# Performance work log

Hardware: AMD Instinct MI355X
Metric: run time of the kernel (lower is better)

Reference implementation:

```python
import jax, jax.numpy as jnp
import numpy as np
from jax import lax

IMG = 1280.0          # image side (80 * stride 16)
HF = WF = 80          # feature map
STRIDE = 16
A = 15                # anchors per location (5 sizes x 3 ratios)
KMIX = 5              # MDN mixture components
NIMG = 8
NGT = 32
PRE_NMS = 2000
POST_NMS = 1000
NMS_THRESH = 0.7
BATCH_PER_IMG = 256
POS_FRAC = 0.5
SCALE_CLAMP = float(np.log(1000.0 / 16.0))
LOG2PI = float(np.log(2.0 * np.pi))


def _make_anchors():
    sizes = np.array([32., 64., 128., 256., 512.])
    ratios = np.array([0.5, 1.0, 2.0])
    ws = (sizes[:, None] * np.sqrt(1.0 / ratios)[None, :]).reshape(-1)
    hs = (sizes[:, None] * np.sqrt(ratios)[None, :]).reshape(-1)
    base = np.stack([-ws / 2, -hs / 2, ws / 2, hs / 2], 1)  # [A,4]
    xs = (np.arange(WF) + 0.5) * STRIDE
    ys = (np.arange(HF) + 0.5) * STRIDE
    sx, sy = np.meshgrid(xs, ys)
    shifts = np.stack([sx.ravel(), sy.ravel(), sx.ravel(), sy.ravel()], 1)  # [HW,4]
    return jnp.asarray((shifts[:, None, :] + base[None]).reshape(-1, 4), jnp.float32)


def setup_inputs() -> dict:
    key = jax.random.key(0)
    k = jax.random.split(key, 6)
    R = HF * WF * A
    anchors = _make_anchors()                                                # [R,4]
    pi = jax.random.normal(k[0], (NIMG, KMIX, R), jnp.float32)
    mu = jax.random.normal(k[1], (NIMG, KMIX, R), jnp.float32)
    sigma = jax.random.uniform(k[2], (NIMG, KMIX, R), jnp.float32, 0.1, 1.0)
    deltas = jax.random.normal(k[3], (NIMG, R, 4), jnp.float32) * 0.1
    xy = jax.random.uniform(k[4], (NIMG, NGT, 2), jnp.float32, 0.0, 960.0)
    wh = jax.random.uniform(k[5], (NIMG, NGT, 2), jnp.float32, 20.0, 320.0)
    gt_boxes = jnp.concatenate([xy, xy + wh], -1)                            # [N,G,4]
    return {"anchors": anchors, "pi": pi, "mu": mu, "sigma": sigma,
            "deltas": deltas, "gt_boxes": gt_boxes}


def pairwise_iou(a, b):  # [M,4],[P,4] -> [M,P]
    area_a = (a[:, 2] - a[:, 0]) * (a[:, 3] - a[:, 1])
    area_b = (b[:, 2] - b[:, 0]) * (b[:, 3] - b[:, 1])
    lt = jnp.maximum(a[:, None, :2], b[None, :, :2])
    rb = jnp.minimum(a[:, None, 2:], b[None, :, 2:])
    wh = jnp.clip(rb - lt, 0.0)
    inter = wh[..., 0] * wh[..., 1]
    return inter / jnp.maximum(area_a[:, None] + area_b[None, :] - inter, 1e-9)


def apply_deltas(d, boxes):  # Box2BoxTransform.apply_deltas, weights=(1,1,1,1)
    w = boxes[:, 2] - boxes[:, 0]
    h = boxes[:, 3] - boxes[:, 1]
    cx = boxes[:, 0] + 0.5 * w
    cy = boxes[:, 1] + 0.5 * h
    dx, dy = d[:, 0], d[:, 1]
    dw = jnp.minimum(d[:, 2], SCALE_CLAMP)
    dh = jnp.minimum(d[:, 3], SCALE_CLAMP)
    pcx = dx * w + cx
    pcy = dy * h + cy
    pw = jnp.exp(dw) * w
    ph = jnp.exp(dh) * h
    return jnp.stack([pcx - 0.5 * pw, pcy - 0.5 * ph, pcx + 0.5 * pw, pcy + 0.5 * ph], 1)


def get_deltas(src, tgt):  # Box2BoxTransform.get_deltas
    sw = src[..., 2] - src[..., 0]
    sh = src[..., 3] - src[..., 1]
    scx = src[..., 0] + 0.5 * sw
    scy = src[..., 1] + 0.5 * sh
    tw = tgt[..., 2] - tgt[..., 0]
    th = tgt[..., 3] - tgt[..., 1]
    tcx = tgt[..., 0] + 0.5 * tw
    tcy = tgt[..., 1] + 0.5 * th
    return jnp.stack([(tcx - scx) / sw, (tcy - scy) / sh,
                      jnp.log(tw / sw), jnp.log(th / sh)], -1)


def _nms_image(boxes, scores, unc):  # [R,4],[R],[R,2] -> padded top proposals
    top_s, tidx = lax.top_k(scores, PRE_NMS)
    tb = jnp.clip(boxes[tidx], 0.0, IMG)   # clip to image
    tu = unc[tidx]
    iou = pairwise_iou(tb, tb)             # [PRE,PRE]
    ar = jnp.arange(PRE_NMS)

    def body(i, keep):
        sup = (iou[i] > NMS_THRESH) & (ar > i) & keep[i]
        return keep & ~sup

    keep = lax.fori_loop(0, PRE_NMS, body, jnp.ones((PRE_NMS,), bool))
    wv = tb[:, 2] - tb[:, 0]
    hv = tb[:, 3] - tb[:, 1]
    keep = keep & (wv > 0.0) & (hv > 0.0)  # min_box_size = 0
    ms = jnp.where(keep, top_s, -jnp.inf)
    out_s, oidx = lax.top_k(ms, POST_NMS)
    return tb[oidx], out_s, tu[oidx]


def _losses(anchors, pi, mu, sigma, deltas, gt_boxes):
    # label_and_sample_anchors (no_grad in torch)
    iou = lax.stop_gradient(jax.vmap(lambda g: pairwise_iou(g, anchors))(gt_boxes))  # [N,G,R]
    vals = iou.max(axis=1)                       # matched IoU quality  [N,R]
    idx = jnp.argmax(iou, axis=1)                # matched gt index     [N,R]
    labels = jnp.where(vals >= 0.7, 1, jnp.where(vals >= 0.3, -1, 0))
    best_gt = iou.max(axis=2)                    # [N,G]
    lq = jnp.any((iou >= best_gt[:, :, None] - 1e-7) & (best_gt[:, :, None] > 0), axis=1)
    labels = jnp.where(lq, 1, labels)            # allow_low_quality_matches
    # deterministic subsample to batch_size_per_image with positive_fraction
    pos = labels == 1
    neg = labels == 0
    n_pos = jnp.minimum(pos.sum(1), int(BATCH_PER_IMG * POS_FRAC))
    keep_pos = pos & (jnp.cumsum(pos, 1) <= n_pos[:, None])
    keep_neg = neg & (jnp.cumsum(neg, 1) <= (BATCH_PER_IMG - n_pos)[:, None])
    labels = jnp.where(keep_pos, 1, jnp.where(keep_neg, 0, -1))
    matched_gt = lax.stop_gradient(jax.vmap(lambda g, i: g[i])(gt_boxes, idx))  # [N,R,4]
    gt_deltas = get_deltas(lax.stop_gradient(anchors)[None], matched_gt)
    pos_mask = labels == 1
    # smooth_l1 with beta=0 -> L1, summed over positives
    loss_loc = jnp.sum(jnp.abs(deltas - gt_deltas) * pos_mask[..., None])
    valid = labels != -1
    t = jnp.clip(vals, 0.0, 1.0)
    lp = jax.nn.log_softmax(pi, axis=1)
    comp = lp - 0.5 * ((t[:, None, :] - mu) / sigma) ** 2 - jnp.log(sigma) - 0.5 * LOG2PI
    nll = -jax.nn.logsumexp(comp, axis=1)        # [N,R]
    loss_cls = jnp.sum(nll * valid)
    norm = BATCH_PER_IMG * pi.shape[0]
    return jnp.stack([loss_cls / norm, loss_loc / norm])


def reference(anchors, pi, mu, sigma, deltas, gt_boxes):
    # find_logit: pi-weighted mixture mean as objectness score
    pi_sm = jax.nn.softmax(pi, axis=1)           # [N,K,R]
    logits = jnp.sum(pi_sm * mu, axis=1)         # [N,R]
    # mdn_uncertainties: epistemic / aleatoric
    epis = jnp.sum(pi_sm * (mu - logits[:, None, :]) ** 2, axis=1)
    alea = jnp.sum(pi_sm * sigma ** 2, axis=1)
    unc = jnp.stack([epis, alea], -1)            # [N,R,2]
    # _decode_proposals
    boxes = jax.vmap(lambda d: apply_deltas(d, anchors))(deltas)  # [N,R,4]
    # find_top_rpn_proposals_uncertainty (pre-NMS topk, clip, NMS, post-NMS topk)
    prop_b, prop_s, prop_u = jax.vmap(_nms_image)(boxes, logits, unc)
    losses = _losses(anchors, pi, mu, sigma, deltas, gt_boxes)    # [loss_cls, loss_loc]
    return prop_b, prop_s, prop_u, losses
```

## Files before the change

kernel.cpp:

```cpp
#include <hip/hip_runtime.h>
#include <cstdint>
#include <cstddef>

typedef unsigned long long u64;
typedef unsigned int u32;
typedef unsigned short u16;
typedef unsigned char u8;

#define R_ANCH 96000
#define NIMG   8
#define KMIX   5
#define PRE    2000
#define POST   1000
#define NGT    32
#define NCHUNK 375
#define NBLK   48
#define MROW   2048
#define GC_STRIDE 16
#define SCAP   16
#define BIG_TH 64

#define IMG_SZ        1280.0f
#define NMS_T         0.7f
#define SCALE_CLAMP_F 4.135166556742356f
#define HALF_L2PI     0.9189385332046727f

__device__ __forceinline__ u64 make_key(float s, int r) {
  u32 u = __float_as_uint(s);
  u = (u & 0x80000000u) ? ~u : (u | 0x80000000u);
  return ((u64)u << 32) | (u64)(0xFFFFFFFFu - (u32)r);
}

__device__ __forceinline__ float dec_score(u64 key) {
  u32 o = (u32)(key >> 32);
  u32 bits = (o & 0x80000000u) ? (o ^ 0x80000000u) : ~o;
  return __uint_as_float(bits);
}

__device__ __forceinline__ float iou_pair(float a0,float a1,float a2,float a3,
                                          float b0,float b1,float b2,float b3) {
#pragma clang fp contract(off)
  float areaA = (a2-a0)*(a3-a1);
  float areaB = (b2-b0)*(b3-b1);
  float lx=fmaxf(a0,b0), ly=fmaxf(a1,b1);
  float rx=fminf(a2,b2), ry=fminf(a3,b3);
  float iw=fmaxf(rx-lx,0.0f), ih=fmaxf(ry-ly,0.0f);
  float inter=iw*ih;
  return inter / fmaxf(areaA+areaB-inter, 1e-9f);
}

__device__ __forceinline__ void pick2048(const u32* __restrict__ hist, int k,
                                         int* s_i, u32* s_u,
                                         int& d_out, int& k_out, u32& cnt_out) {
  int tid = threadIdx.x;
  int lane = tid & 63, w = tid >> 6;
  u32 h[8]; u32 ssum = 0;
#pragma unroll
  for (int i=0;i<8;++i){ h[i] = hist[2047 - (tid*8 + i)]; ssum += h[i]; }
  u32 incl = ssum;
  for (int off=1; off<64; off<<=1){
    u32 t = (u32)__shfl_up((int)incl, off, 64);
    if (lane >= off) incl += t;
  }
  if (lane==63) s_i[w] = (int)incl;
  __syncthreads();
  u32 base = 0;
  for (int ww=0; ww<w; ++ww) base += (u32)s_i[ww];
  u32 run = base + incl - ssum;
#pragma unroll
  for (int i=0;i<8;++i){
    u32 nr = run + h[i];
    if (run < (u32)k && nr >= (u32)k){
      s_u[0] = (u32)(2047 - (tid*8+i));
      s_u[1] = (u32)k - run;
      s_u[2] = h[i];
    }
    run = nr;
  }
  __syncthreads();
  d_out = (int)s_u[0]; k_out = (int)s_u[1]; cnt_out = s_u[2];
  __syncthreads();
}

__device__ __forceinline__ void scan2048_desc(const u32* __restrict__ h,
                                              u32* __restrict__ off,
                                              u32* __restrict__ wsum, int tid) {
  int b_hi = 2047 - 2*tid, b_lo = b_hi - 1;
  u32 h_hi = h[b_hi], h_lo = h[b_lo];
  u32 sum = h_hi + h_lo;
  u32 incl = sum;
  int lane = tid & 63, wv = tid >> 6;
  for (int o=1; o<64; o<<=1){
    u32 t = (u32)__shfl_up((int)incl, o, 64);
    if (lane >= o) incl += t;
  }
  if (lane==63) wsum[wv] = incl;
  __syncthreads();
  u32 base = 0;
  for (int w=0; w<wv; ++w) base += wsum[w];
  u32 excl = base + incl - sum;
  off[b_hi] = excl;
  off[b_lo] = excl + h_hi;
}

__global__ void kZero(u32* z, int nwords) {
  for (int i = blockIdx.x*256 + threadIdx.x; i < nwords; i += gridDim.x*256)
    z[i] = 0u;
}

__global__ __launch_bounds__(256) void kA_mdn(
    const float* __restrict__ pi, const float* __restrict__ mu,
    const float* __restrict__ sigma, float* __restrict__ logits,
    float* __restrict__ epis, float* __restrict__ alea,
    u32* __restrict__ hist0,
    const float* __restrict__ anchors, const float* __restrict__ gt,
    const float* __restrict__ deltas,
    float* __restrict__ nll_o, float* __restrict__ loc_o) {
  __shared__ u32 s_h[2048];
  __shared__ float s_gt[NGT*4];
  int tid = threadIdx.x;
  int r = blockIdx.x*256 + tid;
  int img = blockIdx.y;
  for (int b=tid; b<2048; b+=256) s_h[b]=0u;
  if (tid < NGT*4) s_gt[tid] = gt[img*NGT*4 + tid];
  size_t base = (size_t)img*KMIX*R_ANCH + r;
  float p[KMIX], m[KMIX], s[KMIX];
#pragma unroll
  for (int k=0;k<KMIX;k++){
    p[k]=pi[base+(size_t)k*R_ANCH];
    m[k]=mu[base+(size_t)k*R_ANCH];
    s[k]=sigma[base+(size_t)k*R_ANCH];
  }
  float mx = p[0];
#pragma unroll
  for (int k=1;k<KMIX;k++) mx = fmaxf(mx,p[k]);
  float e[KMIX]; float sum = 0.0f;
#pragma unroll
  for (int k=0;k<KMIX;k++){ e[k]=expf(p[k]-mx); sum += e[k]; }
  float w[KMIX]; float lg = 0.0f;
#pragma unroll
  for (int k=0;k<KMIX;k++){ w[k]=e[k]/sum; lg += w[k]*m[k]; }
  float ep = 0.0f, al = 0.0f;
#pragma unroll
  for (int k=0;k<KMIX;k++){ float d=m[k]-lg; ep += w[k]*d*d; al += w[k]*s[k]*s[k]; }
  size_t o = (size_t)img*R_ANCH + r;
  logits[o]=lg; epis[o]=ep; alea[o]=al;
  __syncthreads();
  u64 key = make_key(lg, r);
  atomicAdd(&s_h[(u32)(key>>53)], 1u);
  float4 a = ((const float4*)anchors)[r];
  float aA = (a.z-a.x)*(a.w-a.y);
  float bi = -1.0f, bu = 1.0f; int idx = 0;
#pragma unroll 4
  for (int g=0; g<NGT; ++g){
    float g0=s_gt[g*4], g1=s_gt[g*4+1], g2=s_gt[g*4+2], g3=s_gt[g*4+3];
    float ga=(g2-g0)*(g3-g1);
    float lx=fmaxf(g0,a.x), ly=fmaxf(g1,a.y);
    float rx=fminf(g2,a.z), ry=fminf(g3,a.w);
    float iw=fmaxf(rx-lx,0.0f), ih=fmaxf(ry-ly,0.0f);
    float inter=iw*ih;
    float uni = fmaxf(ga + aA - inter, 1e-9f);
    if (inter*bu > bi*uni){ bi=inter; bu=uni; idx=g; }
  }
  float vbest = bi/bu;
  float lsum = logf(sum);
  float t_ = fminf(fmaxf(vbest, 0.0f), 1.0f);
  float comp[KMIX];
#pragma unroll
  for (int k=0;k<KMIX;k++){
    float z = (t_ - m[k]) / s[k];
    comp[k] = (p[k]-mx-lsum) - 0.5f*z*z - logf(s[k]) - HALF_L2PI;
  }
  float cm = comp[0];
#pragma unroll
  for (int k=1;k<KMIX;k++) cm = fmaxf(cm, comp[k]);
  float se = 0.0f;
#pragma unroll
  for (int k=0;k<KMIX;k++) se += expf(comp[k]-cm);
  float nll = -(cm + logf(se));
  const float* gb = &s_gt[idx*4];
  float sw = a.z-a.x, sh = a.w-a.y;
  float scx = a.x+0.5f*sw, scy = a.y+0.5f*sh;
  float tw = gb[2]-gb[0], th = gb[3]-gb[1];
  float tcx = gb[0]+0.5f*tw, tcy = gb[1]+0.5f*th;
  float4 d = ((const float4*)deltas)[(size_t)img*R_ANCH + r];
  float loc = fabsf(d.x-(tcx-scx)/sw) + fabsf(d.y-(tcy-scy)/sh)
            + fabsf(d.z-logf(tw/sw)) + fabsf(d.w-logf(th/sh));
  nll_o[o] = nll; loc_o[o] = loc;
  __syncthreads();
  for (int b=tid; b<2048; b+=256){ u32 v=s_h[b]; if(v) atomicAdd(&hist0[img*2048+b], v); }
}

__global__ __launch_bounds__(256) void kL1_bestgt(const float* __restrict__ anchors,
                                                  const float* __restrict__ gt,
                                                  int* __restrict__ best) {
  __shared__ float s_gt[NGT*4];
  __shared__ float s_ga[NGT];
  __shared__ int s_best[NGT];
  int tid = threadIdx.x, img = blockIdx.y;
  if (tid < NGT*4) s_gt[tid] = gt[img*NGT*4 + tid];
  if (tid < NGT){
    const float* g4 = gt + img*NGT*4 + tid*4;
    s_ga[tid] = (g4[2]-g4[0])*(g4[3]-g4[1]);
    s_best[tid] = 0;
  }
  __syncthreads();
  float4 an[8]; float aA[8];
#pragma unroll
  for (int q=0; q<8; ++q){
    int r = blockIdx.x*256 + tid + q*(NBLK*256);
    an[q] = (r < R_ANCH) ? ((const float4*)anchors)[r]
                         : make_float4(0.f,0.f,0.f,0.f);
    aA[q] = (an[q].z-an[q].x)*(an[q].w-an[q].y);
  }
  float vmax[NGT];
#pragma unroll 2
  for (int g=0; g<NGT; ++g){
    float g0=s_gt[g*4], g1=s_gt[g*4+1], g2=s_gt[g*4+2], g3=s_gt[g*4+3];
    float ga=s_ga[g];
    float bi=0.0f, bu=1.0f;
#pragma unroll
    for (int q=0; q<8; ++q){
      float lx=fmaxf(g0,an[q].x), ly=fmaxf(g1,an[q].y);
      float rx=fminf(g2,an[q].z), ry=fminf(g3,an[q].w);
      float iw=fmaxf(rx-lx,0.0f), ih=fmaxf(ry-ly,0.0f);
      float inter=iw*ih;
      float uni=fmaxf(ga+aA[q]-inter,1e-9f);
      if (inter*bu > bi*uni){ bi=inter; bu=uni; }
    }
    vmax[g] = bi/bu;
  }
  int lane = tid & 63;
#pragma unroll
  for (int g=0; g<NGT; ++g){
    float v = vmax[g];
    v = fmaxf(v, __shfl_xor(v, 1, 64));
    v = fmaxf(v, __shfl_xor(v, 2, 64));
    v = fmaxf(v, __shfl_xor(v, 4, 64));
    v = fmaxf(v, __shfl_xor(v, 8, 64));
    v = fmaxf(v, __shfl_xor(v,16, 64));
    v = fmaxf(v, __shfl_xor(v,32, 64));
    if (lane==0 && v > 0.0f) atomicMax(&s_best[g], __float_as_int(v));
  }
  __syncthreads();
  if (tid < NGT) atomicMax(&best[img*NGT + tid], s_best[tid]);
}

__global__ __launch_bounds__(256) void kP1(const float* __restrict__ logits,
                                           const u32* __restrict__ hist0,
                                           u32* __restrict__ hist1) {
  __shared__ u32 s_h[2048];
  __shared__ int s_i[8]; __shared__ u32 s_u[3];
  int img = blockIdx.y, tid = threadIdx.x;
  int d0,k0; u32 c0;
  pick2048(hist0 + img*2048, PRE, s_i, s_u, d0,k0,c0);
  if (c0 <= 2048u) return;
  for (int b=tid; b<2048; b+=256) s_h[b]=0u;
  __syncthreads();
  const float* sc = logits + (size_t)img*R_ANCH;
  for (int r = blockIdx.x*256 + tid; r < R_ANCH; r += NBLK*256){
    u64 key = make_key(sc[r], r);
    if ((int)(key>>53) == d0) atomicAdd(&s_h[(u32)(key>>42)&2047u], 1u);
  }
  __syncthreads();
  for (int b=tid; b<2048; b+=256){ u32 v=s_h[b]; if(v) atomicAdd(&hist1[img*2048+b], v); }
}

__global__ __launch_bounds__(256) void kP2(const float* __restrict__ logits,
                                           const u32* __restrict__ hist0,
                                           const u32* __restrict__ hist1,
                                           u32* __restrict__ hist2) {
  __shared__ u32 s_h[2048];
  __shared__ int s_i[8]; __shared__ u32 s_u[3];
  int img = blockIdx.y, tid = threadIdx.x;
  int d0,k0; u32 c0;
  pick2048(hist0 + img*2048, PRE, s_i, s_u, d0,k0,c0);
  if (c0 <= 2048u) return;
  int d1,k1; u32 c1;
  pick2048(hist1 + img*2048, k0, s_i, s_u, d1,k1,c1);
  if (c1 <= 2048u) return;
  u64 p1 = ((u64)d0<<11) | (u64)d1;
  for (int b=tid; b<2048; b+=256) s_h[b]=0u;
  __syncthreads();
  const float* sc = logits + (size_t)img*R_ANCH;
  for (int r = blockIdx.x*256 + tid; r < R_ANCH; r += NBLK*256){
    u64 key = make_key(sc[r], r);
    if ((key>>42) == p1) atomicAdd(&s_h[(u32)(key>>31)&2047u], 1u);
  }
  __syncthreads();
  for (int b=tid; b<2048; b+=256){ u32 v=s_h[b]; if(v) atomicAdd(&hist2[img*2048+b], v); }
}

__global__ __launch_bounds__(256) void kGather(const float* __restrict__ logits,
    const u32* __restrict__ hist0, const u32* __restrict__ hist1,
    const u32* __restrict__ hist2, u64* __restrict__ cand, u32* __restrict__ gcnt) {
  __shared__ int s_i[8]; __shared__ u32 s_u[3];
  __shared__ u64 s_cand[2048];
  __shared__ u32 s_cnt, s_base;
  int img = blockIdx.y, tid = threadIdx.x;
  if (tid==0) s_cnt = 0u;
  int d,kk; u32 c;
  pick2048(hist0 + img*2048, PRE, s_i, s_u, d,kk,c);
  u64 p = (u64)d; int L = 0;
  if (c > 2048u){
    pick2048(hist1 + img*2048, kk, s_i, s_u, d,kk,c);
    p = (p<<11)|(u64)d; L = 1;
    if (c > 2048u){
      pick2048(hist2 + img*2048, kk, s_i, s_u, d,kk,c);
      p = (p<<11)|(u64)d; L = 2;
    }
  }
  u64 T = p << (64 - 11*(L+1));
  const float* sc = logits + (size_t)img*R_ANCH;
  int lane = tid & 63;
  for (int r = blockIdx.x*256 + tid; r < R_ANCH; r += NBLK*256){
    u64 key = make_key(sc[r], r);
    bool take = (key >= T);
    u64 b = __ballot(take);
    if (b){
      u32 base = 0;
      if (lane==0) base = atomicAdd(&s_cnt, (u32)__popcll(b));
      base = (u32)__shfl((int)base, 0, 64);
      if (take){
        u32 pos = base + (u32)__popcll(b & ((1ull<<lane)-1ull));
        if (pos < 2048u) s_cand[pos] = key;
        else {
          u32 gp = atomicAdd(&gcnt[img*GC_STRIDE], 1u);
          if (gp < 4096u) cand[(size_t)img*4096 + gp] = key;
        }
      }
    }
  }
  __syncthreads();
  u32 n = s_cnt < 2048u ? s_cnt : 2048u;
  if (tid==0) s_base = atomicAdd(&gcnt[img*GC_STRIDE], n);
  __syncthreads();
  u32 gb = s_base;
  for (u32 i=tid; i<n; i+=256)
    cand[(size_t)img*4096 + gb + i] = s_cand[i];
}

__global__ __launch_bounds__(1024) void kRank(
    const u64* __restrict__ cand, const u32* __restrict__ gcnt,
    const float* __restrict__ epis, const float* __restrict__ alea,
    const float* __restrict__ deltas, const float* __restrict__ anchors,
    float* __restrict__ tb, float* __restrict__ tu, float* __restrict__ ts) {
  __shared__ u64 s_key[4096];
  __shared__ u16 s_idx0[4096];
  __shared__ u16 s_idx1[4096];
  __shared__ u32 s_h0[2048];
  __shared__ u32 s_off0[2048];
  __shared__ u32 s_h1[2048];
  __shared__ u32 s_off1[2048];
  __shared__ u32 s_wsum[16];
  __shared__ u32 s_nbig;
  __shared__ u16 s_big[64];
  int tid = threadIdx.x, img = blockIdx.x;
  u32 cnt = gcnt[img*GC_STRIDE];
  if (cnt > 4096u) cnt = 4096u;
  const u64* cp = cand + (size_t)img*4096;
  for (int i=tid; i<4096; i+=1024) s_key[i] = (i < (int)cnt) ? cp[i] : 0ull;
  for (int b=tid; b<2048; b+=1024){ s_h0[b] = 0u; }
  if (tid==0) s_nbig = 0u;
  __syncthreads();
  for (int i=tid; i<(int)cnt; i+=1024)
    atomicAdd(&s_h0[(u32)(s_key[i]>>53)], 1u);
  __syncthreads();
  scan2048_desc(s_h0, s_off0, s_wsum, tid);
  __syncthreads();
  for (int b=tid; b<2048; b+=1024){
    u32 sz = s_h0[b];
    if (sz > BIG_TH && s_off0[b] < PRE){
      u32 q = atomicAdd(&s_nbig, 1u);
      if (q < 64u) s_big[q] = (u16)b;
    }
  }
  for (int i=tid; i<(int)cnt; i+=1024){
    u32 d = (u32)(s_key[i]>>53);
    u32 slot = atomicAdd(&s_off0[d], 1u);
    s_idx0[slot] = (u16)i;
  }
  __syncthreads();
  auto emit = [&](u64 my, u32 rank){
    if (rank < PRE){
      int p = (int)rank;
      u32 idx = 0xFFFFFFFFu - (u32)(my & 0xFFFFFFFFull);
      ts[img*PRE + p] = dec_score(my);
      float4 a = ((const float4*)anchors)[idx];
      float4 dd = ((const float4*)deltas)[(size_t)img*R_ANCH + idx];
      float w = a.z - a.x, h = a.w - a.y;
      float cx = a.x + 0.5f*w, cy = a.y + 0.5f*h;
      float dw = fminf(dd.z, SCALE_CLAMP_F), dh = fminf(dd.w, SCALE_CLAMP_F);
      float pcx = dd.x*w + cx, pcy = dd.y*h + cy;
      float pw = expf(dw)*w, ph = expf(dh)*h;
      float x0 = fminf(fmaxf(pcx - 0.5f*pw, 0.0f), IMG_SZ);
      float y0 = fminf(fmaxf(pcy - 0.5f*ph, 0.0f), IMG_SZ);
      float x1 = fminf(fmaxf(pcx + 0.5f*pw, 0.0f), IMG_SZ);
      float y1 = fminf(fmaxf(pcy + 0.5f*ph, 0.0f), IMG_SZ);
      ((float4*)tb)[(size_t)img*PRE + p] = make_float4(x0,y0,x1,y1);
      size_t o = (size_t)img*R_ANCH + idx;
      ((float2*)tu)[(size_t)img*PRE + p] = make_float2(epis[o], alea[o]);
    }
  };
  for (int i=tid; i<(int)cnt; i+=1024){
    u64 my = s_key[i];
    u32 d = (u32)(my>>53);
    u32 size = s_h0[d];
    if (size > BIG_TH) continue;
    u32 bs = s_off0[d] - size;
    if (bs >= PRE) continue;
    u32 rank = bs;
    for (u32 q=bs; q<bs+size; ++q)
      rank += (s_key[s_idx0[q]] > my) ? 1u : 0u;
    emit(my, rank);
  }
  __syncthreads();
  u32 nbig = s_nbig < 64u ? s_nbig : 64u;
  for (u32 bb=0; bb<nbig; ++bb){
    u32 B = s_big[bb];
    u32 size = s_h0[B];
    u32 base0 = s_off0[B] - size;
    for (int b=tid; b<2048; b+=1024) s_h1[b] = 0u;
    __syncthreads();
    for (u32 q=tid; q<size; q+=1024){
      u64 k = s_key[s_idx0[base0+q]];
      atomicAdd(&s_h1[(u32)(k>>42)&2047u], 1u);
    }
    __syncthreads();
    scan2048_desc(s_h1, s_off1, s_wsum, tid);
    __syncthreads();
    for (u32 q=tid; q<size; q+=1024){
      u16 ci = s_idx0[base0+q];
      u64 k = s_key[ci];
      u32 slot = atomicAdd(&s_off1[(u32)(k>>42)&2047u], 1u);
      s_idx1[slot] = ci;
    }
    __syncthreads();
    for (u32 q=tid; q<size; q+=1024){
      u16 ci = s_idx1[q];
      u64 my = s_key[ci];
      u32 d1 = (u32)(my>>42)&2047u;
      u32 ssz = s_h1[d1];
      u32 sbs = s_off1[d1] - ssz;
      u32 rank = base0 + sbs;
      for (u32 t2=sbs; t2<sbs+ssz; ++t2)
        rank += (s_key[s_idx1[t2]] > my) ? 1u : 0u;
      emit(my, rank);
    }
    __syncthreads();
  }
}

__global__ __launch_bounds__(1024) void kD_mask(const float* __restrict__ tb,
                                                u64* __restrict__ maskLT,
                                                u32* __restrict__ scnt,
                                                u16* __restrict__ slist) {
  __shared__ float4 s_tile[64];
  int tid = threadIdx.x;
  int a = blockIdx.x, img = blockIdx.y;
  const float4* tbi = (const float4*)tb + (size_t)img*PRE;
  if (tid < 64){
    int i = a*64 + tid;
    s_tile[tid] = (i < PRE) ? tbi[i] : make_float4(0.f,0.f,0.f,0.f);
  }
  __syncthreads();
  u64* outp = maskLT + ((size_t)img*32 + a)*MROW;
  u32* cnts = scnt + (size_t)img*2048;
  u16* lst  = slist + (size_t)img*2048*SCAP;
  int bmax = min(64, PRE - a*64);
  for (int j = a*64 + tid; j < MROW; j += 1024){
    u64 m = 0ull;
    if (j < PRE){
      float4 B = tbi[j];
      int blim = min(bmax, j - a*64);
      for (int b = 0; b < blim; ++b){
        float4 A = s_tile[b];
        float v = iou_pair(A.x,A.y,A.z,A.w, B.x,B.y,B.z,B.w);
        m |= (u64)(v > NMS_T) << b;
      }
    }
    outp[j] = m;
    u64 mm = m;
    while (mm){
      int b = __builtin_ctzll(mm); mm &= mm - 1ull;
      u32 slot = atomicAdd(&cnts[j], 1u);
      if (slot < SCAP) lst[(size_t)j*SCAP + slot] = (u16)(a*64 + b);
    }
  }
}

__global__ __launch_bounds__(1024) void kE_nms(const u64* __restrict__ maskLT,
                                               const u32* __restrict__ scnt,
                                               const u16* __restrict__ slist,
                                               u64* __restrict__ keep) {
  __shared__ u64 s_list64[2048*SCAP/4];
  __shared__ u16 s_cnt[2048];
  __shared__ u8  kbuf[2][2048];
  __shared__ u64 s_kw[32];
  __shared__ int s_change, s_ovf;
  int img = blockIdx.x, tid = threadIdx.x;
  const u64* gl = (const u64*)(slist + (size_t)img*2048*SCAP);
  for (int i=tid; i<2048*SCAP/4; i+=1024) s_list64[i] = gl[i];
  const u32* gc = scnt + (size_t)img*2048;
  for (int i=tid; i<2048; i+=1024) s_cnt[i] = (u16)gc[i];
  if (tid==0){ s_change = 0; s_ovf = 0; }
  __syncthreads();
  bool myovf = false;
#pragma unroll
  for (int q=0; q<2; ++q){
    int j = tid + q*1024;
    if (s_cnt[j] > SCAP) myovf = true;
    kbuf[0][j] = (j < PRE) ? 1 : 0;
  }
  if (myovf) s_ovf = 1;
  __syncthreads();
  const u64* MT = maskLT + (size_t)img*32*MROW;
  int cur = 0;
  for (int iter=0; iter<2048; ++iter){
    bool ovf = (s_ovf != 0);
    if (ovf && tid < 32){
      u64 w = 0ull;
      for (int b=0; b<64; ++b) w |= (u64)(kbuf[cur][tid*64+b] & 1) << b;
      s_kw[tid] = w;
    }
    __syncthreads();
    bool changed = false;
#pragma unroll
    for (int q=0; q<2; ++q){
      int j = tid + q*1024;
      u8 old = kbuf[cur][j];
      u8 nk = (j < PRE) ? 1 : 0;
      if (nk){
        int cnt = s_cnt[j];
        if (cnt <= SCAP){
          const u16* lp = (const u16*)&s_list64[j*(SCAP/4)];
          for (int i=0; i<cnt; ++i){
            if (kbuf[cur][lp[i]]){ nk = 0; break; }
          }
        } else {
          int amax = j >> 6;
          for (int a=0; a<=amax; ++a){
            if (MT[(size_t)a*MROW + j] & s_kw[a]){ nk = 0; break; }
          }
        }
      }
      kbuf[1-cur][j] = nk;
      changed |= (nk != old);
    }
    if (changed) s_change = 1;
    __syncthreads();
    int ch = s_change;
    __syncthreads();
    if (tid==0) s_change = 0;
    if (!ch) break;
    cur ^= 1;
  }
  if (tid < 32){
    u64 w = 0ull;
    for (int b=0; b<64; ++b) w |= (u64)(kbuf[cur][tid*64+b] & 1) << b;
    keep[img*32 + tid] = w;
  }
}

__global__ __launch_bounds__(256) void kL2_label(
    const float* __restrict__ anchors, const float* __restrict__ gt,
    const int* __restrict__ best,
    signed char* __restrict__ label, int* __restrict__ cpos, int* __restrict__ cneg) {
  __shared__ float s_gt[NGT*4];
  __shared__ float s_ga[NGT];
  __shared__ float s_bg[NGT];
  __shared__ int s_w[8];
  int tid = threadIdx.x, img = blockIdx.y;
  int r = blockIdx.x*256 + tid;
  if (tid < NGT*4) s_gt[tid] = gt[img*NGT*4 + tid];
  if (tid < NGT){
    const float* g4 = gt + img*NGT*4 + tid*4;
    s_ga[tid] = (g4[2]-g4[0])*(g4[3]-g4[1]);
    s_bg[tid] = __int_as_float(best[img*NGT + tid]);
  }
  __syncthreads();
  float4 a = ((const float4*)anchors)[r];
  float aA = (a.z-a.x)*(a.w-a.y);
  float bi=-1.0f, bu=1.0f; bool lq = false;
#pragma unroll 4
  for (int g=0; g<NGT; ++g){
    float g0=s_gt[g*4], g1=s_gt[g*4+1], g2=s_gt[g*4+2], g3=s_gt[g*4+3];
    float lx=fmaxf(g0,a.x), ly=fmaxf(g1,a.y);
    float rx=fminf(g2,a.z), ry=fminf(g3,a.w);
    float iw=fmaxf(rx-lx,0.0f), ih=fmaxf(ry-ly,0.0f);
    float inter=iw*ih;
    float uni = fmaxf(s_ga[g] + aA - inter, 1e-9f);
    if (inter*bu > bi*uni){ bi=inter; bu=uni; }
    float bg = s_bg[g];
    lq = lq || ((inter >= (bg - 1e-7f)*uni) && (bg > 0.0f));
  }
  float vbest = bi/bu;
  int lab = lq ? 1 : (vbest >= 0.7f ? 1 : (vbest >= 0.3f ? -1 : 0));
  label[(size_t)img*R_ANCH + r] = (signed char)lab;
  u64 bp = __ballot(lab==1), bn = __ballot(lab==0);
  int wid = tid>>6, lane = tid&63;
  if (lane==0){ s_w[wid*2]=__popcll(bp); s_w[wid*2+1]=__popcll(bn); }
  __syncthreads();
  if (tid==0){
    cpos[img*NCHUNK + blockIdx.x] = s_w[0]+s_w[2]+s_w[4]+s_w[6];
    cneg[img*NCHUNK + blockIdx.x] = s_w[1]+s_w[3]+s_w[5]+s_w[7];
  }
}

__global__ __launch_bounds__(512) void kL3_scan(const int* __restrict__ cpos,
                                                const int* __restrict__ cneg,
                                                int* __restrict__ opos,
                                                int* __restrict__ oneg,
                                                int* __restrict__ quota) {
  __shared__ int s_p[8], s_n[8];
  int img = blockIdx.x, tid = threadIdx.x;
  int vp=0, vn=0;
  if (tid < NCHUNK){ vp = cpos[img*NCHUNK+tid]; vn = cneg[img*NCHUNK+tid]; }
  int lane = tid&63, w = tid>>6;
  int ip=vp, in_=vn;
  for (int off=1; off<64; off<<=1){
    int tp=__shfl_up(ip,off,64), tn=__shfl_up(in_,off,64);
    if (lane>=off){ ip+=tp; in_+=tn; }
  }
  if (lane==63){ s_p[w]=ip; s_n[w]=in_; }
  __syncthreads();
  int bp=0,bn=0;
  for (int ww=0; ww<w; ++ww){ bp+=s_p[ww]; bn+=s_n[ww]; }
  if (tid < NCHUNK){
    opos[img*NCHUNK+tid] = bp+ip-vp;
    oneg[img*NCHUNK+tid] = bn+in_-vn;
  }
  if (tid==0){
    int tp=0,tn=0;
    for (int ww=0; ww<8; ++ww){ tp+=s_p[ww]; tn+=s_n[ww]; }
    int np = tp<128?tp:128;
    quota[img*2]=np; quota[img*2+1]=256-np;
  }
}

__global__ __launch_bounds__(256) void kL4_accum(
    const signed char* __restrict__ label, const float* __restrict__ nll_i,
    const float* __restrict__ loc_i, const int* __restrict__ opos,
    const int* __restrict__ oneg, const int* __restrict__ quota,
    float* __restrict__ acc) {
  __shared__ int s_wp[4], s_wn[4];
  __shared__ float s_red[8];
  int tid = threadIdx.x, img = blockIdx.y;
  int r = blockIdx.x*256 + tid;
  size_t o = (size_t)img*R_ANCH + r;
  int lab = label[o];
  bool pos = (lab==1), neg = (lab==0);
  u64 bp = __ballot(pos), bn = __ballot(neg);
  int wid = tid>>6, lane = tid&63;
  if (lane==0){ s_wp[wid]=__popcll(bp); s_wn[wid]=__popcll(bn); }
  __syncthreads();
  int pre_p = opos[img*NCHUNK + blockIdx.x];
  int pre_n = oneg[img*NCHUNK + blockIdx.x];
  for (int w=0; w<wid; ++w){ pre_p += s_wp[w]; pre_n += s_wn[w]; }
  u64 lm = (1ull<<lane) - 1ull;
  pre_p += __popcll(bp & lm);
  pre_n += __popcll(bn & lm);
  int np = quota[img*2], nn = quota[img*2+1];
  bool kp = pos && (pre_p < np);
  bool kn = neg && (pre_n < nn);
  float c_cls = (kp||kn) ? nll_i[o] : 0.0f;
  float c_loc = kp ? loc_i[o] : 0.0f;
  for (int of=32; of>0; of>>=1){
    c_cls += __shfl_down(c_cls, of, 64);
    c_loc += __shfl_down(c_loc, of, 64);
  }
  if (lane==0){ s_red[wid]=c_cls; s_red[4+wid]=c_loc; }
  __syncthreads();
  if (tid==0){
    float a = s_red[0]+s_red[1]+s_red[2]+s_red[3];
    float b = s_red[4]+s_red[5]+s_red[6]+s_red[7];
    if (a != 0.0f) atomicAdd(&acc[0], a);
    if (b != 0.0f) atomicAdd(&acc[1], b);
  }
}

__global__ __launch_bounds__(256) void kF_final(
    const float* __restrict__ tb, const float* __restrict__ tu,
    const float* __restrict__ ts, const u64* __restrict__ keepw,
    const float* __restrict__ acc, float* __restrict__ out) {
  __shared__ int s_wk[4], s_wn[4];
  __shared__ int s_kc, s_runk, s_runn;
  int tid = threadIdx.x, img = blockIdx.x;
  int wid = tid>>6, lane = tid&63;
  const u64* kw = keepw + img*32;
  const float NEG_INF = __uint_as_float(0xff800000u);
  int cnt = 0;
  for (int c=0; c<8; ++c){
    int p = c*256 + tid;
    float4 b = ((const float4*)tb)[(size_t)img*PRE + p];
    bool kp = (p < PRE) && (((kw[p>>6]>>(p&63))&1ull)!=0ull) && (b.z > b.x) && (b.w > b.y);
    cnt += kp ? 1 : 0;
  }
  for (int of=32; of>0; of>>=1) cnt += __shfl_down(cnt, of, 64);
  if (lane==0) s_wk[wid] = cnt;
  __syncthreads();
  if (tid==0){ s_kc = s_wk[0]+s_wk[1]+s_wk[2]+s_wk[3]; s_runk=0; s_runn=0; }
  __syncthreads();
  int kc = s_kc;
  for (int c=0; c<8; ++c){
    int p = c*256 + tid;
    float4 b = ((const float4*)tb)[(size_t)img*PRE + p];
    bool kp = (p < PRE) && (((kw[p>>6]>>(p&63))&1ull)!=0ull) && (b.z > b.x) && (b.w > b.y);
    u64 bk = __ballot(kp), bn = __ballot(!kp);
    if (lane==0){ s_wk[wid]=__popcll(bk); s_wn[wid]=__popcll(bn); }
    __syncthreads();
    int pk = s_runk, pn = s_runn;
    for (int w=0; w<wid; ++w){ pk += s_wk[w]; pn += s_wn[w]; }
    u64 lm = (1ull<<lane) - 1ull;
    pk += __popcll(bk & lm);
    pn += __popcll(bn & lm);
    int slot = kp ? pk : (kc + pn);
    if (slot < POST && p < PRE){
      ((float4*)out)[img*POST + slot] = b;
      out[32000 + img*POST + slot] = kp ? ts[img*PRE + p] : NEG_INF;
      ((float2*)(out + 40000))[img*POST + slot] = ((const float2*)tu)[(size_t)img*PRE + p];
    }
    __syncthreads();
    if (tid==0){
      s_runk += s_wk[0]+s_wk[1]+s_wk[2]+s_wk[3];
      s_runn += s_wn[0]+s_wn[1]+s_wn[2]+s_wn[3];
    }
    __syncthreads();
  }
  if (img==0 && tid<2) out[56000+tid] = acc[tid] * (1.0f/2048.0f);
}

extern "C" void kernel_launch(void* const* d_in, const int* in_sizes, int n_in,
                              void* d_out, int out_size, void* d_ws, size_t ws_size,
                              hipStream_t stream) {
  const float* anchors = (const float*)d_in[0];
  const float* pi      = (const float*)d_in[1];
  const float* mu      = (const float*)d_in[2];
  const float* sigma   = (const float*)d_in[3];
  const float* deltas  = (const float*)d_in[4];
  const float* gt      = (const float*)d_in[5];
  float* out = (float*)d_out;

  char* ws = (char*)d_ws;
  size_t off = 0;
  auto alloc = [&](size_t bytes) -> void* {
    void* p = (void*)(ws + off);
    off += (bytes + 255) & ~(size_t)255;
    return p;
  };
  float* logits = (float*)alloc((size_t)NIMG*R_ANCH*4);
  float* epis   = (float*)alloc((size_t)NIMG*R_ANCH*4);
  float* alea   = (float*)alloc((size_t)NIMG*R_ANCH*4);
  float* nll    = (float*)alloc((size_t)NIMG*R_ANCH*4);
  float* loc    = (float*)alloc((size_t)NIMG*R_ANCH*4);
  float* tb     = (float*)alloc((size_t)NIMG*PRE*4*4);
  float* tu     = (float*)alloc((size_t)NIMG*PRE*2*4);
  float* ts     = (float*)alloc((size_t)NIMG*PRE*4);
  u64*   maskLT = (u64*)  alloc((size_t)NIMG*32*MROW*8);
  u16*   slist  = (u16*)  alloc((size_t)NIMG*2048*SCAP*2);
  u64*   keepw  = (u64*)  alloc((size_t)NIMG*32*8);
  u64*   cand   = (u64*)  alloc((size_t)NIMG*4096*8);
  int*   cpos   = (int*)  alloc((size_t)NIMG*NCHUNK*4);
  int*   cneg   = (int*)  alloc((size_t)NIMG*NCHUNK*4);
  int*   opos   = (int*)  alloc((size_t)NIMG*NCHUNK*4);
  int*   oneg   = (int*)  alloc((size_t)NIMG*NCHUNK*4);
  int*   quota  = (int*)  alloc((size_t)NIMG*2*4);
  size_t zstart = off;
  u32*   hist0  = (u32*)  alloc((size_t)NIMG*2048*4);
  u32*   hist1  = (u32*)  alloc((size_t)NIMG*2048*4);
  u32*   hist2  = (u32*)  alloc((size_t)NIMG*2048*4);
  u32*   gcnt   = (u32*)  alloc((size_t)NIMG*GC_STRIDE*4);
  int*   best   = (int*)  alloc((size_t)NIMG*NGT*4);
  u32*   scnt   = (u32*)  alloc((size_t)NIMG*2048*4);
  float* acc    = (float*)alloc(8);
  int zwords = (int)((off - zstart) / 4);
  signed char* label = (signed char*)logits;

  kZero<<<dim3(64), dim3(256), 0, stream>>>((u32*)(ws + zstart), zwords);
  kA_mdn<<<dim3(NCHUNK, NIMG), dim3(256), 0, stream>>>(pi, mu, sigma, logits, epis, alea,
                                                       hist0, anchors, gt, deltas, nll, loc);
  kL1_bestgt<<<dim3(NBLK, NIMG), dim3(256), 0, stream>>>(anchors, gt, best);
  kP1<<<dim3(NBLK, NIMG), dim3(256), 0, stream>>>(logits, hist0, hist1);
  kP2<<<dim3(NBLK, NIMG), dim3(256), 0, stream>>>(logits, hist0, hist1, hist2);
  kGather<<<dim3(NBLK, NIMG), dim3(256), 0, stream>>>(logits, hist0, hist1, hist2, cand, gcnt);
  kRank<<<dim3(NIMG), dim3(1024), 0, stream>>>(cand, gcnt, epis, alea, deltas, anchors, tb, tu, ts);
  kD_mask<<<dim3(32, NIMG), dim3(1024), 0, stream>>>(tb, maskLT, scnt, slist);
  kE_nms<<<dim3(NIMG), dim3(1024), 0, stream>>>(maskLT, scnt, slist, keepw);
  kL2_label<<<dim3(NCHUNK, NIMG), dim3(256), 0, stream>>>(anchors, gt, best, label, cpos, cneg);
  kL3_scan<<<dim3(NIMG), dim3(512), 0, stream>>>(cpos, cneg, opos, oneg, quota);
  kL4_accum<<<dim3(NCHUNK, NIMG), dim3(256), 0, stream>>>(label, nll, loc, opos, oneg, quota, acc);
  kF_final<<<dim3(NIMG), dim3(256), 0, stream>>>(tb, tu, ts, keepw, acc, out);
}
```

Measured before the change: 280.7 us.

## Fuse pipeline kernels to cut launch count from thirteen to seven

The best-GT IoU pass is folded into the MDN kernel as extra blocks. The multi-pass radix top-k select (P1, P2, Gather) is merged into the single-block-per-image rank kernel, the label prefix scan is recomputed inside the accumulation kernel, and final compaction moves into the NMS kernel. The goal is to remove launch and inter-kernel serialization overhead and some global round trips. In exchange, the radix refinement passes now run on only 8 blocks (one per image) scanning 96000 logits each, and every accumulation block redundantly re-sums the chunk counts.

```diff
diff --git a/kernel.cpp b/kernel.cpp
--- a/kernel.cpp
+++ b/kernel.cpp
@@ -16,7 +16,6 @@
 #define NCHUNK 375
 #define NBLK   48
 #define MROW   2048
-#define GC_STRIDE 16
 #define SCAP   16
 #define BIG_TH 64
 
@@ -47,39 +46,6 @@
   float iw=fmaxf(rx-lx,0.0f), ih=fmaxf(ry-ly,0.0f);
   float inter=iw*ih;
   return inter / fmaxf(areaA+areaB-inter, 1e-9f);
-}
-
-__device__ __forceinline__ void pick2048(const u32* __restrict__ hist, int k,
-                                         int* s_i, u32* s_u,
-                                         int& d_out, int& k_out, u32& cnt_out) {
-  int tid = threadIdx.x;
-  int lane = tid & 63, w = tid >> 6;
-  u32 h[8]; u32 ssum = 0;
-#pragma unroll
-  for (int i=0;i<8;++i){ h[i] = hist[2047 - (tid*8 + i)]; ssum += h[i]; }
-  u32 incl = ssum;
-  for (int off=1; off<64; off<<=1){
-    u32 t = (u32)__shfl_up((int)incl, off, 64);
-    if (lane >= off) incl += t;
-  }
-  if (lane==63) s_i[w] = (int)incl;
-  __syncthreads();
-  u32 base = 0;
-  for (int ww=0; ww<w; ++ww) base += (u32)s_i[ww];
-  u32 run = base + incl - ssum;
-#pragma unroll
-  for (int i=0;i<8;++i){
-    u32 nr = run + h[i];
-    if (run < (u32)k && nr >= (u32)k){
-      s_u[0] = (u32)(2047 - (tid*8+i));
-      s_u[1] = (u32)k - run;
-      s_u[2] = h[i];
-    }
-    run = nr;
-  }
-  __syncthreads();
-  d_out = (int)s_u[0]; k_out = (int)s_u[1]; cnt_out = s_u[2];
-  __syncthreads();
 }
 
 __device__ __forceinline__ void scan2048_desc(const u32* __restrict__ h,
@@ -115,12 +81,67 @@
     u32* __restrict__ hist0,
     const float* __restrict__ anchors, const float* __restrict__ gt,
     const float* __restrict__ deltas,
-    float* __restrict__ nll_o, float* __restrict__ loc_o) {
+    float* __restrict__ nll_o, float* __restrict__ loc_o,
+    int* __restrict__ best) {
   __shared__ u32 s_h[2048];
   __shared__ float s_gt[NGT*4];
+  __shared__ float s_ga[NGT];
+  __shared__ int s_best[NGT];
   int tid = threadIdx.x;
+  int img = blockIdx.y;
+
+  if (blockIdx.x >= NCHUNK) {
+    int bx = blockIdx.x - NCHUNK;
+    if (tid < NGT*4) s_gt[tid] = gt[img*NGT*4 + tid];
+    if (tid < NGT){
+      const float* g4 = gt + img*NGT*4 + tid*4;
+      s_ga[tid] = (g4[2]-g4[0])*(g4[3]-g4[1]);
+      s_best[tid] = 0;
+    }
+    __syncthreads();
+    float4 an[8]; float aA[8];
+#pragma unroll
+    for (int q=0; q<8; ++q){
+      int r = bx*256 + tid + q*(NBLK*256);
+      an[q] = (r < R_ANCH) ? ((const float4*)anchors)[r]
+                           : make_float4(0.f,0.f,0.f,0.f);
+      aA[q] = (an[q].z-an[q].x)*(an[q].w-an[q].y);
+    }
+    float vmax[NGT];
+#pragma unroll 2
+    for (int g=0; g<NGT; ++g){
+      float g0=s_gt[g*4], g1=s_gt[g*4+1], g2=s_gt[g*4+2], g3=s_gt[g*4+3];
+      float ga=s_ga[g];
+      float bi=0.0f, bu=1.0f;
+#pragma unroll
+      for (int q=0; q<8; ++q){
+        float lx=fmaxf(g0,an[q].x), ly=fmaxf(g1,an[q].y);
+        float rx=fminf(g2,an[q].z), ry=fminf(g3,an[q].w);
+        float iw=fmaxf(rx-lx,0.0f), ih=fmaxf(ry-ly,0.0f);
+        float inter=iw*ih;
+        float uni=fmaxf(ga+aA[q]-inter,1e-9f);
+        if (inter*bu > bi*uni){ bi=inter; bu=uni; }
+      }
+      vmax[g] = bi/bu;
+    }
+    int lane = tid & 63;
+#pragma unroll
+    for (int g=0; g<NGT; ++g){
+      float v = vmax[g];
+      v = fmaxf(v, __shfl_xor(v, 1, 64));
+      v = fmaxf(v, __shfl_xor(v, 2, 64));
+      v = fmaxf(v, __shfl_xor(v, 4, 64));
+      v = fmaxf(v, __shfl_xor(v, 8, 64));
+      v = fmaxf(v, __shfl_xor(v,16, 64));
+      v = fmaxf(v, __shfl_xor(v,32, 64));
+      if (lane==0 && v > 0.0f) atomicMax(&s_best[g], __float_as_int(v));
+    }
+    __syncthreads();
+    if (tid < NGT) atomicMax(&best[img*NGT + tid], s_best[tid]);
+    return;
+  }
+
   int r = blockIdx.x*256 + tid;
-  int img = blockIdx.y;
   for (int b=tid; b<2048; b+=256) s_h[b]=0u;
   if (tid < NGT*4) s_gt[tid] = gt[img*NGT*4 + tid];
   size_t base = (size_t)img*KMIX*R_ANCH + r;
@@ -191,157 +212,8 @@
   for (int b=tid; b<2048; b+=256){ u32 v=s_h[b]; if(v) atomicAdd(&hist0[img*2048+b], v); }
 }
 
-__global__ __launch_bounds__(256) void kL1_bestgt(const float* __restrict__ anchors,
-                                                  const float* __restrict__ gt,
-                                                  int* __restrict__ best) {
-  __shared__ float s_gt[NGT*4];
-  __shared__ float s_ga[NGT];
-  __shared__ int s_best[NGT];
-  int tid = threadIdx.x, img = blockIdx.y;
-  if (tid < NGT*4) s_gt[tid] = gt[img*NGT*4 + tid];
-  if (tid < NGT){
-    const float* g4 = gt + img*NGT*4 + tid*4;
-    s_ga[tid] = (g4[2]-g4[0])*(g4[3]-g4[1]);
-    s_best[tid] = 0;
-  }
-  __syncthreads();
-  float4 an[8]; float aA[8];
-#pragma unroll
-  for (int q=0; q<8; ++q){
-    int r = blockIdx.x*256 + tid + q*(NBLK*256);
-    an[q] = (r < R_ANCH) ? ((const float4*)anchors)[r]
-                         : make_float4(0.f,0.f,0.f,0.f);
-    aA[q] = (an[q].z-an[q].x)*(an[q].w-an[q].y);
-  }
-  float vmax[NGT];
-#pragma unroll 2
-  for (int g=0; g<NGT; ++g){
-    float g0=s_gt[g*4], g1=s_gt[g*4+1], g2=s_gt[g*4+2], g3=s_gt[g*4+3];
-    float ga=s_ga[g];
-    float bi=0.0f, bu=1.0f;
-#pragma unroll
-    for (int q=0; q<8; ++q){
-      float lx=fmaxf(g0,an[q].x), ly=fmaxf(g1,an[q].y);
-      float rx=fminf(g2,an[q].z), ry=fminf(g3,an[q].w);
-      float iw=fmaxf(rx-lx,0.0f), ih=fmaxf(ry-ly,0.0f);
-      float inter=iw*ih;
-      float uni=fmaxf(ga+aA[q]-inter,1e-9f);
-      if (inter*bu > bi*uni){ bi=inter; bu=uni; }
-    }
-    vmax[g] = bi/bu;
-  }
-  int lane = tid & 63;
-#pragma unroll
-  for (int g=0; g<NGT; ++g){
-    float v = vmax[g];
-    v = fmaxf(v, __shfl_xor(v, 1, 64));
-    v = fmaxf(v, __shfl_xor(v, 2, 64));
-    v = fmaxf(v, __shfl_xor(v, 4, 64));
-    v = fmaxf(v, __shfl_xor(v, 8, 64));
-    v = fmaxf(v, __shfl_xor(v,16, 64));
-    v = fmaxf(v, __shfl_xor(v,32, 64));
-    if (lane==0 && v > 0.0f) atomicMax(&s_best[g], __float_as_int(v));
-  }
-  __syncthreads();
-  if (tid < NGT) atomicMax(&best[img*NGT + tid], s_best[tid]);
-}
-
-__global__ __launch_bounds__(256) void kP1(const float* __restrict__ logits,
-                                           const u32* __restrict__ hist0,
-                                           u32* __restrict__ hist1) {
-  __shared__ u32 s_h[2048];
-  __shared__ int s_i[8]; __shared__ u32 s_u[3];
-  int img = blockIdx.y, tid = threadIdx.x;
-  int d0,k0; u32 c0;
-  pick2048(hist0 + img*2048, PRE, s_i, s_u, d0,k0,c0);
-  if (c0 <= 2048u) return;
-  for (int b=tid; b<2048; b+=256) s_h[b]=0u;
-  __syncthreads();
-  const float* sc = logits + (size_t)img*R_ANCH;
-  for (int r = blockIdx.x*256 + tid; r < R_ANCH; r += NBLK*256){
-    u64 key = make_key(sc[r], r);
-    if ((int)(key>>53) == d0) atomicAdd(&s_h[(u32)(key>>42)&2047u], 1u);
-  }
-  __syncthreads();
-  for (int b=tid; b<2048; b+=256){ u32 v=s_h[b]; if(v) atomicAdd(&hist1[img*2048+b], v); }
-}
-
-__global__ __launch_bounds__(256) void kP2(const float* __restrict__ logits,
-                                           const u32* __restrict__ hist0,
-                                           const u32* __restrict__ hist1,
-                                           u32* __restrict__ hist2) {
-  __shared__ u32 s_h[2048];
-  __shared__ int s_i[8]; __shared__ u32 s_u[3];
-  int img = blockIdx.y, tid = threadIdx.x;
-  int d0,k0; u32 c0;
-  pick2048(hist0 + img*2048, PRE, s_i, s_u, d0,k0,c0);
-  if (c0 <= 2048u) return;
-  int d1,k1; u32 c1;
-  pick2048(hist1 + img*2048, k0, s_i, s_u, d1,k1,c1);
-  if (c1 <= 2048u) return;
-  u64 p1 = ((u64)d0<<11) | (u64)d1;
-  for (int b=tid; b<2048; b+=256) s_h[b]=0u;
-  __syncthreads();
-  const float* sc = logits + (size_t)img*R_ANCH;
-  for (int r = blockIdx.x*256 + tid; r < R_ANCH; r += NBLK*256){
-    u64 key = make_key(sc[r], r);
-    if ((key>>42) == p1) atomicAdd(&s_h[(u32)(key>>31)&2047u], 1u);
-  }
-  __syncthreads();
-  for (int b=tid; b<2048; b+=256){ u32 v=s_h[b]; if(v) atomicAdd(&hist2[img*2048+b], v); }
-}
-
-__global__ __launch_bounds__(256) void kGather(const float* __restrict__ logits,
-    const u32* __restrict__ hist0, const u32* __restrict__ hist1,
-    const u32* __restrict__ hist2, u64* __restrict__ cand, u32* __restrict__ gcnt) {
-  __shared__ int s_i[8]; __shared__ u32 s_u[3];
-  __shared__ u64 s_cand[2048];
-  __shared__ u32 s_cnt, s_base;
-  int img = blockIdx.y, tid = threadIdx.x;
-  if (tid==0) s_cnt = 0u;
-  int d,kk; u32 c;
-  pick2048(hist0 + img*2048, PRE, s_i, s_u, d,kk,c);
-  u64 p = (u64)d; int L = 0;
-  if (c > 2048u){
-    pick2048(hist1 + img*2048, kk, s_i, s_u, d,kk,c);
-    p = (p<<11)|(u64)d; L = 1;
-    if (c > 2048u){
-      pick2048(hist2 + img*2048, kk, s_i, s_u, d,kk,c);
-      p = (p<<11)|(u64)d; L = 2;
-    }
-  }
-  u64 T = p << (64 - 11*(L+1));
-  const float* sc = logits + (size_t)img*R_ANCH;
-  int lane = tid & 63;
-  for (int r = blockIdx.x*256 + tid; r < R_ANCH; r += NBLK*256){
-    u64 key = make_key(sc[r], r);
-    bool take = (key >= T);
-    u64 b = __ballot(take);
-    if (b){
-      u32 base = 0;
-      if (lane==0) base = atomicAdd(&s_cnt, (u32)__popcll(b));
-      base = (u32)__shfl((int)base, 0, 64);
-      if (take){
-        u32 pos = base + (u32)__popcll(b & ((1ull<<lane)-1ull));
-        if (pos < 2048u) s_cand[pos] = key;
-        else {
-          u32 gp = atomicAdd(&gcnt[img*GC_STRIDE], 1u);
-          if (gp < 4096u) cand[(size_t)img*4096 + gp] = key;
-        }
-      }
-    }
-  }
-  __syncthreads();
-  u32 n = s_cnt < 2048u ? s_cnt : 2048u;
-  if (tid==0) s_base = atomicAdd(&gcnt[img*GC_STRIDE], n);
-  __syncthreads();
-  u32 gb = s_base;
-  for (u32 i=tid; i<n; i+=256)
-    cand[(size_t)img*4096 + gb + i] = s_cand[i];
-}
-
-__global__ __launch_bounds__(1024) void kRank(
-    const u64* __restrict__ cand, const u32* __restrict__ gcnt,
+__global__ __launch_bounds__(1024) void kSelRank(
+    const float* __restrict__ logits, const u32* __restrict__ hist0,
     const float* __restrict__ epis, const float* __restrict__ alea,
     const float* __restrict__ deltas, const float* __restrict__ anchors,
     float* __restrict__ tb, float* __restrict__ tu, float* __restrict__ ts) {
@@ -353,14 +225,71 @@
   __shared__ u32 s_h1[2048];
   __shared__ u32 s_off1[2048];
   __shared__ u32 s_wsum[16];
-  __shared__ u32 s_nbig;
+  __shared__ u32 s_u[3];
+  __shared__ u32 s_nbig, s_cnt;
   __shared__ u16 s_big[64];
   int tid = threadIdx.x, img = blockIdx.x;
-  u32 cnt = gcnt[img*GC_STRIDE];
-  if (cnt > 4096u) cnt = 4096u;
-  const u64* cp = cand + (size_t)img*4096;
-  for (int i=tid; i<4096; i+=1024) s_key[i] = (i < (int)cnt) ? cp[i] : 0ull;
-  for (int b=tid; b<2048; b+=1024){ s_h0[b] = 0u; }
+  const float* sc = logits + (size_t)img*R_ANCH;
+
+  auto pick = [&](u32* h, u32* off, int k){
+    __syncthreads();
+    scan2048_desc(h, off, s_wsum, tid);
+    __syncthreads();
+    int b0 = tid*2;
+    for (int b=b0; b<b0+2; ++b){
+      u32 o = off[b], hh = h[b];
+      if (o < (u32)k && (u32)k <= o + hh){ s_u[0]=(u32)b; s_u[1]=(u32)k - o; s_u[2]=hh; }
+    }
+    __syncthreads();
+  };
+
+  for (int b=tid; b<2048; b+=1024) s_h0[b] = hist0[img*2048 + b];
+  if (tid==0) s_cnt = 0u;
+  pick(s_h0, s_off0, PRE);
+  int d = (int)s_u[0]; int krem = (int)s_u[1]; u32 c = s_u[2];
+  u64 p = (u64)d; int L = 0;
+  if (c > 2048u){
+    for (int b=tid; b<2048; b+=1024) s_h1[b] = 0u;
+    __syncthreads();
+    for (int r=tid; r<R_ANCH; r+=1024){
+      u64 key = make_key(sc[r], r);
+      if ((int)(key>>53) == d) atomicAdd(&s_h1[(u32)(key>>42)&2047u], 1u);
+    }
+    pick(s_h1, s_off1, krem);
+    d = (int)s_u[0]; krem = (int)s_u[1]; c = s_u[2];
+    p = (p<<11) | (u64)d; L = 1;
+    if (c > 2048u){
+      for (int b=tid; b<2048; b+=1024) s_h1[b] = 0u;
+      __syncthreads();
+      for (int r=tid; r<R_ANCH; r+=1024){
+        u64 key = make_key(sc[r], r);
+        if ((key>>42) == p) atomicAdd(&s_h1[(u32)(key>>31)&2047u], 1u);
+      }
+      pick(s_h1, s_off1, krem);
+      d = (int)s_u[0]; krem = (int)s_u[1]; c = s_u[2];
+      p = (p<<11) | (u64)d; L = 2;
+    }
+  }
+  u64 T = p << (64 - 11*(L+1));
+  int lane = tid & 63;
+  for (int r=tid; r<R_ANCH; r+=1024){
+    u64 key = make_key(sc[r], r);
+    bool take = (key >= T);
+    u64 b = __ballot(take);
+    if (b){
+      u32 base = 0;
+      if (lane==0) base = atomicAdd(&s_cnt, (u32)__popcll(b));
+      base = (u32)__shfl((int)base, 0, 64);
+      if (take){
+        u32 pos = base + (u32)__popcll(b & ((1ull<<lane)-1ull));
+        if (pos < 4096u) s_key[pos] = key;
+      }
+    }
+  }
+  __syncthreads();
+  u32 cnt = s_cnt; if (cnt > 4096u) cnt = 4096u;
+
+  for (int b=tid; b<2048; b+=1024) s_h0[b] = 0u;
   if (tid==0) s_nbig = 0u;
   __syncthreads();
   for (int i=tid; i<(int)cnt; i+=1024)
@@ -375,17 +304,18 @@
       if (q < 64u) s_big[q] = (u16)b;
     }
   }
+  __syncthreads();
   for (int i=tid; i<(int)cnt; i+=1024){
-    u32 d = (u32)(s_key[i]>>53);
-    u32 slot = atomicAdd(&s_off0[d], 1u);
+    u32 dd = (u32)(s_key[i]>>53);
+    u32 slot = atomicAdd(&s_off0[dd], 1u);
     s_idx0[slot] = (u16)i;
   }
   __syncthreads();
   auto emit = [&](u64 my, u32 rank){
     if (rank < PRE){
-      int p = (int)rank;
+      int pp = (int)rank;
       u32 idx = 0xFFFFFFFFu - (u32)(my & 0xFFFFFFFFull);
-      ts[img*PRE + p] = dec_score(my);
+      ts[img*PRE + pp] = dec_score(my);
       float4 a = ((const float4*)anchors)[idx];
       float4 dd = ((const float4*)deltas)[(size_t)img*R_ANCH + idx];
       float w = a.z - a.x, h = a.w - a.y;
@@ -397,17 +327,17 @@
       float y0 = fminf(fmaxf(pcy - 0.5f*ph, 0.0f), IMG_SZ);
       float x1 = fminf(fmaxf(pcx + 0.5f*pw, 0.0f), IMG_SZ);
       float y1 = fminf(fmaxf(pcy + 0.5f*ph, 0.0f), IMG_SZ);
-      ((float4*)tb)[(size_t)img*PRE + p] = make_float4(x0,y0,x1,y1);
+      ((float4*)tb)[(size_t)img*PRE + pp] = make_float4(x0,y0,x1,y1);
       size_t o = (size_t)img*R_ANCH + idx;
-      ((float2*)tu)[(size_t)img*PRE + p] = make_float2(epis[o], alea[o]);
+      ((float2*)tu)[(size_t)img*PRE + pp] = make_float2(epis[o], alea[o]);
     }
   };
   for (int i=tid; i<(int)cnt; i+=1024){
     u64 my = s_key[i];
-    u32 d = (u32)(my>>53);
-    u32 size = s_h0[d];
+    u32 dd = (u32)(my>>53);
+    u32 size = s_h0[dd];
     if (size > BIG_TH) continue;
-    u32 bs = s_off0[d] - size;
+    u32 bs = s_off0[dd] - size;
     if (bs >= PRE) continue;
     u32 rank = bs;
     for (u32 q=bs; q<bs+size; ++q)
@@ -489,16 +419,20 @@
   }
 }
 
-__global__ __launch_bounds__(1024) void kE_nms(const u64* __restrict__ maskLT,
-                                               const u32* __restrict__ scnt,
-                                               const u16* __restrict__ slist,
-                                               u64* __restrict__ keep) {
+__global__ __launch_bounds__(1024) void kEF_nms(const u64* __restrict__ maskLT,
+    const u32* __restrict__ scnt, const u16* __restrict__ slist,
+    const float* __restrict__ tb, const float* __restrict__ tu,
+    const float* __restrict__ ts, const float* __restrict__ acc,
+    float* __restrict__ out) {
   __shared__ u64 s_list64[2048*SCAP/4];
   __shared__ u16 s_cnt[2048];
   __shared__ u8  kbuf[2][2048];
   __shared__ u64 s_kw[32];
   __shared__ int s_change, s_ovf;
+  __shared__ int s_wk[16], s_wn[16];
+  __shared__ int s_kc, s_runk, s_runn;
   int img = blockIdx.x, tid = threadIdx.x;
+  int lane = tid & 63, wid = tid >> 6;
   const u64* gl = (const u64*)(slist + (size_t)img*2048*SCAP);
   for (int i=tid; i<2048*SCAP/4; i+=1024) s_list64[i] = gl[i];
   const u32* gc = scnt + (size_t)img*2048;
@@ -555,11 +489,60 @@
     if (!ch) break;
     cur ^= 1;
   }
-  if (tid < 32){
-    u64 w = 0ull;
-    for (int b=0; b<64; ++b) w |= (u64)(kbuf[cur][tid*64+b] & 1) << b;
-    keep[img*32 + tid] = w;
-  }
+  __syncthreads();
+  const float4* tbi = (const float4*)tb + (size_t)img*PRE;
+  const float NEG_INF = __uint_as_float(0xff800000u);
+  u8* kf = kbuf[1-cur];
+#pragma unroll
+  for (int cch=0; cch<2; ++cch){
+    int pp = cch*1024 + tid;
+    bool kp = false;
+    if (pp < PRE && kbuf[cur][pp]){
+      float4 b = tbi[pp];
+      kp = (b.z > b.x) && (b.w > b.y);
+    }
+    kf[pp] = kp ? 1 : 0;
+  }
+  __syncthreads();
+  {
+    int cc = (int)kf[tid] + (int)kf[1024 + tid];
+    for (int of=32; of>0; of>>=1) cc += __shfl_down(cc, of, 64);
+    if (lane==0) s_wk[wid] = cc;
+  }
+  __syncthreads();
+  if (tid==0){
+    int t=0; for (int w=0; w<16; ++w) t += s_wk[w];
+    s_kc = t; s_runk = 0; s_runn = 0;
+  }
+  __syncthreads();
+  int kc = s_kc;
+#pragma unroll
+  for (int cch=0; cch<2; ++cch){
+    int pp = cch*1024 + tid;
+    bool kp = kf[pp] != 0;
+    u64 bk = __ballot(kp), bn = __ballot(!kp);
+    if (lane==0){ s_wk[wid]=__popcll(bk); s_wn[wid]=__popcll(bn); }
+    __syncthreads();
+    int pk = s_runk, pn = s_runn;
+    for (int w=0; w<wid; ++w){ pk += s_wk[w]; pn += s_wn[w]; }
+    u64 lm = (1ull<<lane) - 1ull;
+    pk += __popcll(bk & lm);
+    pn += __popcll(bn & lm);
+    int slot = kp ? pk : (kc + pn);
+    if (slot < POST && pp < PRE){
+      ((float4*)out)[img*POST + slot] = tbi[pp];
+      out[32000 + img*POST + slot] = kp ? ts[img*PRE + pp] : NEG_INF;
+      ((float2*)(out + 40000))[img*POST + slot] = ((const float2*)tu)[(size_t)img*PRE + pp];
+    }
+    __syncthreads();
+    if (tid==0){
+      int tk=0, tn=0;
+      for (int w=0; w<16; ++w){ tk += s_wk[w]; tn += s_wn[w]; }
+      s_runk += tk; s_runn += tn;
+    }
+    __syncthreads();
+  }
+  if (img==0 && tid<2) out[56000+tid] = acc[tid] * (1.0f/2048.0f);
 }
 
 __global__ __launch_bounds__(256) void kL2_label(
@@ -607,60 +590,45 @@
   }
 }
 
-__global__ __launch_bounds__(512) void kL3_scan(const int* __restrict__ cpos,
-                                                const int* __restrict__ cneg,
-                                                int* __restrict__ opos,
-                                                int* __restrict__ oneg,
-                                                int* __restrict__ quota) {
-  __shared__ int s_p[8], s_n[8];
-  int img = blockIdx.x, tid = threadIdx.x;
-  int vp=0, vn=0;
-  if (tid < NCHUNK){ vp = cpos[img*NCHUNK+tid]; vn = cneg[img*NCHUNK+tid]; }
-  int lane = tid&63, w = tid>>6;
-  int ip=vp, in_=vn;
-  for (int off=1; off<64; off<<=1){
-    int tp=__shfl_up(ip,off,64), tn=__shfl_up(in_,off,64);
-    if (lane>=off){ ip+=tp; in_+=tn; }
-  }
-  if (lane==63){ s_p[w]=ip; s_n[w]=in_; }
-  __syncthreads();
-  int bp=0,bn=0;
-  for (int ww=0; ww<w; ++ww){ bp+=s_p[ww]; bn+=s_n[ww]; }
-  if (tid < NCHUNK){
-    opos[img*NCHUNK+tid] = bp+ip-vp;
-    oneg[img*NCHUNK+tid] = bn+in_-vn;
-  }
-  if (tid==0){
-    int tp=0,tn=0;
-    for (int ww=0; ww<8; ++ww){ tp+=s_p[ww]; tn+=s_n[ww]; }
-    int np = tp<128?tp:128;
-    quota[img*2]=np; quota[img*2+1]=256-np;
-  }
-}
-
 __global__ __launch_bounds__(256) void kL4_accum(
     const signed char* __restrict__ label, const float* __restrict__ nll_i,
-    const float* __restrict__ loc_i, const int* __restrict__ opos,
-    const int* __restrict__ oneg, const int* __restrict__ quota,
-    float* __restrict__ acc) {
+    const float* __restrict__ loc_i, const int* __restrict__ cpos,
+    const int* __restrict__ cneg, float* __restrict__ acc) {
   __shared__ int s_wp[4], s_wn[4];
+  __shared__ int s_r[12];
   __shared__ float s_red[8];
-  int tid = threadIdx.x, img = blockIdx.y;
-  int r = blockIdx.x*256 + tid;
+  int tid = threadIdx.x, img = blockIdx.y, bx = blockIdx.x;
+  int lane = tid & 63, wid = tid >> 6;
+  int vp=0, vn=0, tp=0;
+  for (int k=tid; k<NCHUNK; k+=256){
+    int cp = cpos[img*NCHUNK + k];
+    int cn = cneg[img*NCHUNK + k];
+    tp += cp;
+    if (k < bx){ vp += cp; vn += cn; }
+  }
+  for (int of=32; of>0; of>>=1){
+    vp += __shfl_down(vp, of, 64);
+    vn += __shfl_down(vn, of, 64);
+    tp += __shfl_down(tp, of, 64);
+  }
+  if (lane==0){ s_r[wid]=vp; s_r[4+wid]=vn; s_r[8+wid]=tp; }
+  __syncthreads();
+  int pre_p = s_r[0]+s_r[1]+s_r[2]+s_r[3];
+  int pre_n = s_r[4]+s_r[5]+s_r[6]+s_r[7];
+  int totp  = s_r[8]+s_r[9]+s_r[10]+s_r[11];
+  int np = totp < 128 ? totp : 128;
+  int nn = 256 - np;
+  int r = bx*256 + tid;
   size_t o = (size_t)img*R_ANCH + r;
   int lab = label[o];
   bool pos = (lab==1), neg = (lab==0);
   u64 bp = __ballot(pos), bn = __ballot(neg);
-  int wid = tid>>6, lane = tid&63;
   if (lane==0){ s_wp[wid]=__popcll(bp); s_wn[wid]=__popcll(bn); }
   __syncthreads();
-  int pre_p = opos[img*NCHUNK + blockIdx.x];
-  int pre_n = oneg[img*NCHUNK + blockIdx.x];
   for (int w=0; w<wid; ++w){ pre_p += s_wp[w]; pre_n += s_wn[w]; }
   u64 lm = (1ull<<lane) - 1ull;
   pre_p += __popcll(bp & lm);
   pre_n += __popcll(bn & lm);
-  int np = quota[img*2], nn = quota[img*2+1];
   bool kp = pos && (pre_p < np);
   bool kn = neg && (pre_n < nn);
   float c_cls = (kp||kn) ? nll_i[o] : 0.0f;
@@ -677,57 +645,6 @@
     if (a != 0.0f) atomicAdd(&acc[0], a);
     if (b != 0.0f) atomicAdd(&acc[1], b);
   }
-}
-
-__global__ __launch_bounds__(256) void kF_final(
-    const float* __restrict__ tb, const float* __restrict__ tu,
-    const float* __restrict__ ts, const u64* __restrict__ keepw,
-    const float* __restrict__ acc, float* __restrict__ out) {
-  __shared__ int s_wk[4], s_wn[4];
-  __shared__ int s_kc, s_runk, s_runn;
-  int tid = threadIdx.x, img = blockIdx.x;
-  int wid = tid>>6, lane = tid&63;
-  const u64* kw = keepw + img*32;
-  const float NEG_INF = __uint_as_float(0xff800000u);
-  int cnt = 0;
-  for (int c=0; c<8; ++c){
-    int p = c*256 + tid;
-    float4 b = ((const float4*)tb)[(size_t)img*PRE + p];
-    bool kp = (p < PRE) && (((kw[p>>6]>>(p&63))&1ull)!=0ull) && (b.z > b.x) && (b.w > b.y);
-    cnt += kp ? 1 : 0;
-  }
-  for (int of=32; of>0; of>>=1) cnt += __shfl_down(cnt, of, 64);
-  if (lane==0) s_wk[wid] = cnt;
-  __syncthreads();
-  if (tid==0){ s_kc = s_wk[0]+s_wk[1]+s_wk[2]+s_wk[3]; s_runk=0; s_runn=0; }
-  __syncthreads();
-  int kc = s_kc;
-  for (int c=0; c<8; ++c){
-    int p = c*256 + tid;
-    float4 b = ((const float4*)tb)[(size_t)img*PRE + p];
-    bool kp = (p < PRE) && (((kw[p>>6]>>(p&63))&1ull)!=0ull) && (b.z > b.x) && (b.w > b.y);
-    u64 bk = __ballot(kp), bn = __ballot(!kp);
-    if (lane==0){ s_wk[wid]=__popcll(bk); s_wn[wid]=__popcll(bn); }
-    __syncthreads();
-    int pk = s_runk, pn = s_runn;
-    for (int w=0; w<wid; ++w){ pk += s_wk[w]; pn += s_wn[w]; }
-    u64 lm = (1ull<<lane) - 1ull;
-    pk += __popcll(bk & lm);
-    pn += __popcll(bn & lm);
-    int slot = kp ? pk : (kc + pn);
-    if (slot < POST && p < PRE){
-      ((float4*)out)[img*POST + slot] = b;
-      out[32000 + img*POST + slot] = kp ? ts[img*PRE + p] : NEG_INF;
-      ((float2*)(out + 40000))[img*POST + slot] = ((const float2*)tu)[(size_t)img*PRE + p];
-    }
-    __syncthreads();
-    if (tid==0){
-      s_runk += s_wk[0]+s_wk[1]+s_wk[2]+s_wk[3];
-      s_runn += s_wn[0]+s_wn[1]+s_wn[2]+s_wn[3];
-    }
-    __syncthreads();
-  }
-  if (img==0 && tid<2) out[56000+tid] = acc[tid] * (1.0f/2048.0f);
 }
 
 extern "C" void kernel_launch(void* const* d_in, const int* in_sizes, int n_in,
@@ -758,18 +675,10 @@
   float* ts     = (float*)alloc((size_t)NIMG*PRE*4);
   u64*   maskLT = (u64*)  alloc((size_t)NIMG*32*MROW*8);
   u16*   slist  = (u16*)  alloc((size_t)NIMG*2048*SCAP*2);
-  u64*   keepw  = (u64*)  alloc((size_t)NIMG*32*8);
-  u64*   cand   = (u64*)  alloc((size_t)NIMG*4096*8);
   int*   cpos   = (int*)  alloc((size_t)NIMG*NCHUNK*4);
   int*   cneg   = (int*)  alloc((size_t)NIMG*NCHUNK*4);
-  int*   opos   = (int*)  alloc((size_t)NIMG*NCHUNK*4);
-  int*   oneg   = (int*)  alloc((size_t)NIMG*NCHUNK*4);
-  int*   quota  = (int*)  alloc((size_t)NIMG*2*4);
   size_t zstart = off;
   u32*   hist0  = (u32*)  alloc((size_t)NIMG*2048*4);
-  u32*   hist1  = (u32*)  alloc((size_t)NIMG*2048*4);
-  u32*   hist2  = (u32*)  alloc((size_t)NIMG*2048*4);
-  u32*   gcnt   = (u32*)  alloc((size_t)NIMG*GC_STRIDE*4);
   int*   best   = (int*)  alloc((size_t)NIMG*NGT*4);
   u32*   scnt   = (u32*)  alloc((size_t)NIMG*2048*4);
   float* acc    = (float*)alloc(8);
@@ -777,17 +686,11 @@
   signed char* label = (signed char*)logits;
 
   kZero<<<dim3(64), dim3(256), 0, stream>>>((u32*)(ws + zstart), zwords);
-  kA_mdn<<<dim3(NCHUNK, NIMG), dim3(256), 0, stream>>>(pi, mu, sigma, logits, epis, alea,
-                                                       hist0, anchors, gt, deltas, nll, loc);
-  kL1_bestgt<<<dim3(NBLK, NIMG), dim3(256), 0, stream>>>(anchors, gt, best);
-  kP1<<<dim3(NBLK, NIMG), dim3(256), 0, stream>>>(logits, hist0, hist1);
-  kP2<<<dim3(NBLK, NIMG), dim3(256), 0, stream>>>(logits, hist0, hist1, hist2);
-  kGather<<<dim3(NBLK, NIMG), dim3(256), 0, stream>>>(logits, hist0, hist1, hist2, cand, gcnt);
-  kRank<<<dim3(NIMG), dim3(1024), 0, stream>>>(cand, gcnt, epis, alea, deltas, anchors, tb, tu, ts);
+  kA_mdn<<<dim3(NCHUNK+NBLK, NIMG), dim3(256), 0, stream>>>(pi, mu, sigma, logits, epis, alea,
+                                                            hist0, anchors, gt, deltas, nll, loc, best);
+  kSelRank<<<dim3(NIMG), dim3(1024), 0, stream>>>(logits, hist0, epis, alea, deltas, anchors, tb, tu, ts);
   kD_mask<<<dim3(32, NIMG), dim3(1024), 0, stream>>>(tb, maskLT, scnt, slist);
-  kE_nms<<<dim3(NIMG), dim3(1024), 0, stream>>>(maskLT, scnt, slist, keepw);
   kL2_label<<<dim3(NCHUNK, NIMG), dim3(256), 0, stream>>>(anchors, gt, best, label, cpos, cneg);
-  kL3_scan<<<dim3(NIMG), dim3(512), 0, stream>>>(cpos, cneg, opos, oneg, quota);
-  kL4_accum<<<dim3(NCHUNK, NIMG), dim3(256), 0, stream>>>(label, nll, loc, opos, oneg, quota, acc);
-  kF_final<<<dim3(NIMG), dim3(256), 0, stream>>>(tb, tu, ts, keepw, acc, out);
-}
+  kL4_accum<<<dim3(NCHUNK, NIMG), dim3(256), 0, stream>>>(label, nll, loc, cpos, cneg, acc);
+  kEF_nms<<<dim3(NIMG), dim3(1024), 0, stream>>>(maskLT, scnt, slist, tb, tu, ts, acc, out);
+}
```

Result: slower. 322.6 us (+14.9%).
